# Kernel optimization log

Measured on AMD Instinct MI355X. Metric: run time of the kernel, lower is better.

The kernel has to match this reference:

```python
import math
import jax, jax.numpy as jnp
import numpy as np

HID = 2048
H = 16
HKV = 8
D = HID // H          # 128 head_dim
F = D                 # feature_dim = head_dim
SEQ = 2048
BATCH = 2
THETA = 10000.0


def setup_inputs() -> dict:
    key = jax.random.key(0)
    ks = jax.random.split(key, 10)
    s = lambda k, shape, scale=0.02: (jax.random.normal(k, shape, dtype=jnp.float32) * scale)
    return {
        "hidden_states": jax.random.normal(ks[0], (BATCH, SEQ, HID), dtype=jnp.float32),
        "Wq": s(ks[1], (HID, HID)),
        "bq": s(ks[2], (HID,)),
        "Wk": s(ks[3], (HKV * D, HID)),
        "bk": s(ks[4], (HKV * D,)),
        "Wv": s(ks[5], (HKV * D, HID)),
        "bv": s(ks[6], (HKV * D,)),
        "Wo": s(ks[7], (HID, HID)),
        "bo": s(ks[8], (HID,)),
        "rand_matrix": jax.random.normal(ks[9], (F // 2, D), dtype=jnp.float32),
    }


def _rotate_half(x):
    x1, x2 = x[..., : x.shape[-1] // 2], x[..., x.shape[-1] // 2 :]
    return jnp.concatenate((-x2, x1), axis=-1)


def _softmax_kernel(x, R):
    # L2-normalize last dim (norm clamped at 1e-6), project, [sin, cos] features
    n = jnp.sqrt(jnp.sum(x * x, axis=-1, keepdims=True))
    x = x / jnp.maximum(n, 1e-6)
    p = jnp.einsum("...d,ed->...e", x, R)          # [..., F/2]
    feats = jnp.concatenate([jnp.sin(p), jnp.cos(p)], axis=-1)
    return feats / math.sqrt(F)


def reference(hidden_states, Wq, bq, Wk, bk, Wv, bv, Wo, bo, rand_matrix):
    b, s, _ = hidden_states.shape
    q = (hidden_states @ Wq.T + bq).reshape(b, s, H, D).transpose(0, 2, 1, 3)    # bhsd
    k = (hidden_states @ Wk.T + bk).reshape(b, s, HKV, D).transpose(0, 2, 1, 3)
    v = (hidden_states @ Wv.T + bv).reshape(b, s, HKV, D).transpose(0, 2, 1, 3)

    # RoPE (default position_ids = arange)
    inv_freq = 1.0 / (THETA ** (jnp.arange(0, D, 2, dtype=jnp.float32) / D))     # [D/2]
    freqs = jnp.arange(s, dtype=jnp.float32)[:, None] * inv_freq[None, :]        # [s, D/2]
    emb = jnp.concatenate((freqs, freqs), axis=-1)                               # [s, D]
    cos = jnp.cos(emb)[None, None, :, :]
    sin = jnp.sin(emb)[None, None, :, :]
    q = q * cos + _rotate_half(q) * sin
    k = k * cos + _rotate_half(k) * sin

    # GQA repeat (repeat_interleave along head axis)
    rep = H // HKV
    k = jnp.repeat(k, rep, axis=1)
    v = jnp.repeat(v, rep, axis=1)

    qp = _softmax_kernel(q, rand_matrix)   # [b,H,s,F]
    kp = _softmax_kernel(k, rand_matrix)   # [b,H,s,F]

    # Faithful to source einsums: contraction over the HEAD axis
    # torch: 'bsnd,bsnh->bndh' with tensors laid out (b, head, seq, dim)
    kv = jnp.einsum("bhsf,bhsd->bsfd", kp, v)        # [b, s, F, D]
    out = jnp.einsum("bhsf,bsfd->bhsd", qp, kv)      # [b, H, s, D]
    out = out.reshape(b, s, HID)                      # flat reshape, as in source
    return out @ Wo.T + bo
```

## Files before the change

kernel.cpp:

```cpp
#include <hip/hip_runtime.h>
#include <stdint.h>

typedef unsigned short ushort_t;
typedef __bf16 bf16x8 __attribute__((ext_vector_type(8)));
typedef float f32x4 __attribute__((ext_vector_type(4)));
typedef unsigned int u32;

__device__ __forceinline__ float bf2f(ushort_t u) {
    union { u32 u; float f; } x; x.u = ((u32)u) << 16; return x.f;
}
__device__ __forceinline__ ushort_t f2bf(float f) {
    union { float f; u32 u; } x; x.f = f;
    u32 r = x.u + 0x7FFFu + ((x.u >> 16) & 1u);
    return (ushort_t)(r >> 16);
}

__device__ __forceinline__ void async16(const void* gp, void* lp) {
    __builtin_amdgcn_global_load_lds(
        (const __attribute__((address_space(1))) u32*)(gp),
        (__attribute__((address_space(3))) u32*)(lp),
        16, 0, 0);
}

template<int N>
__device__ __forceinline__ void wait_barrier() {
    asm volatile("s_waitcnt vmcnt(%0)\n\ts_barrier" :: "n"(N) : "memory");
}

__global__ __launch_bounds__(256) void cast_all_kernel(
    const float* __restrict__ hs, const float* __restrict__ Wq,
    const float* __restrict__ Wk, const float* __restrict__ Wv,
    const float* __restrict__ Wo, const float* __restrict__ Rm,
    const float* __restrict__ bq, const float* __restrict__ bk,
    const float* __restrict__ bv,
    ushort_t* __restrict__ Xb, ushort_t* __restrict__ Wcat,
    ushort_t* __restrict__ Wo16, ushort_t* __restrict__ Rbf,
    float* __restrict__ bcat)
{
    int bid = blockIdx.x;
    if (bid == 10244) {
        for (int i = threadIdx.x; i < 4096; i += 256) {
            float v = (i < 2048) ? bq[i] : (i < 3072) ? bk[i - 2048] : bv[i - 3072];
            bcat[i] = v;
        }
        return;
    }
    const float* src; ushort_t* dst; int base;
    if (bid < 4096)       { src = hs; dst = Xb;              base = bid; }
    else if (bid < 6144)  { src = Wq; dst = Wcat;            base = bid - 4096; }
    else if (bid < 7168)  { src = Wk; dst = Wcat + 4194304;  base = bid - 6144; }
    else if (bid < 8192)  { src = Wv; dst = Wcat + 6291456;  base = bid - 7168; }
    else if (bid < 10240) { src = Wo; dst = Wo16;            base = bid - 8192; }
    else                  { src = Rm; dst = Rbf;             base = bid - 10240; }
    int i = base * 2048 + threadIdx.x * 8;
    float4 v0 = *reinterpret_cast<const float4*>(src + i);
    float4 v1 = *reinterpret_cast<const float4*>(src + i + 4);
    ushort_t o[8];
    o[0] = f2bf(v0.x); o[1] = f2bf(v0.y); o[2] = f2bf(v0.z); o[3] = f2bf(v0.w);
    o[4] = f2bf(v1.x); o[5] = f2bf(v1.y); o[6] = f2bf(v1.z); o[7] = f2bf(v1.w);
    *reinterpret_cast<uint4*>(dst + i) = *reinterpret_cast<const uint4*>(o);
}

#define CLOSE_PLAIN __builtin_amdgcn_s_barrier()
#define CLOSE_VM(nn) do { asm volatile("s_waitcnt vmcnt(%0)" :: "n"(nn) : "memory"); \
                          __builtin_amdgcn_s_barrier(); } while (0)

template<int BM, int MBLK, int NBLK, int KC, bool STORE_BF16>
__global__ __launch_bounds__(512, 2) void gemm8p_kernel(
    const ushort_t* __restrict__ A, const ushort_t* __restrict__ B,
    const float* __restrict__ bias, void* __restrict__ C,
    const int M, const int N)
{
    constexpr int NT  = KC / 64;
    constexpr int NI  = NT / 2;
    constexpr int MF2 = BM / 64;
    constexpr int NFR = BM / 32;
    constexpr int AH  = BM * 64;
    constexpr int SH  = BM / 128;
    constexpr int BUF = 2 * AH + 32768;
    constexpr int TI  = 2 * SH + 4;
    static_assert(NT % 2 == 0 && NI >= 3, "need even NT >= 6");
    __shared__ alignas(16) char lds[2 * BUF];

    const int tid  = threadIdx.x;
    const int wid  = tid >> 6;
    const int lane = tid & 63;
    const int wm = wid >> 2, wn = wid & 3;

    constexpr int XN  = NBLK / 8;
    constexpr int NXR = 8 / XN;
    constexpr int RH  = MBLK / NXR;
    const int x  = blockIdx.x & 7;
    const int kb = blockIdx.x >> 3;
    const int mb = (x % NXR) * RH + (kb >> 3);
    const int nb = (x / NXR) * 8 + (kb & 7);
    const int am0 = mb * BM, bn0 = nb * 256;

    const int sr3 = tid >> 3;
    const int c8  = tid & 7;
    const int cs  = c8 ^ (sr3 & 7);
    const long K2 = (long)KC * 2;
    const char* agp = (const char*)A + (size_t)(am0 + sr3) * K2 + cs * 16;
    const char* bgp = (const char*)B + (size_t)(bn0 + sr3) * K2 + cs * 16;
    const int ldsw = wid << 10;

    const int fr = lane & 15, fc = lane >> 4;
    const int sw0 = ((fc)     ^ (fr & 7)) * 16;
    const int sw1 = ((4 + fc) ^ (fr & 7)) * 16;
    const int abase = wm * AH + fr * 128;
    const int bbase = 2 * AH + wn * 8192 + fr * 128;

    f32x4 acc[NFR][4] = {};
    bf16x8 bf[4];

    auto stage_half = [&](const char* gp, int rowoff, int bufb, int off,
                          long kof, int niss) {
        char* lp = lds + bufb + off + ldsw;
        const char* g = gp + (size_t)rowoff * K2 + kof;
#pragma unroll
        for (int i = 0; i < niss; ++i)
            async16(g + (size_t)(i * 64) * K2, lp + i * 8192);
    };
#define SA0(T) stage_half(agp, 0,      ((T) & 1) * BUF, 0,          (long)(T) * 128, SH)
#define SA1(T) stage_half(agp, BM / 2, ((T) & 1) * BUF, AH,         (long)(T) * 128, SH)
#define SB0(T) stage_half(bgp, 0,      ((T) & 1) * BUF, 2 * AH,     (long)(T) * 128, 2)
#define SB1(T) stage_half(bgp, 128,    ((T) & 1) * BUF, 2 * AH + 16384, (long)(T) * 128, 2)

#define PH(h, kc, bufb, STG, CLOSE) do {                                      \
    const char* lp_ = lds + (bufb);                                           \
    const int sw_ = (kc) ? sw1 : sw0;                                         \
    if ((h) == 0) {                                                           \
        _Pragma("unroll") for (int n = 0; n < 4; ++n)                         \
            bf[n] = *(const bf16x8*)(lp_ + bbase + n * 2048 + sw_);           \
    }                                                                         \
    bf16x8 af_[MF2];                                                          \
    _Pragma("unroll") for (int j = 0; j < MF2; ++j)                           \
        af_[j] = *(const bf16x8*)(lp_ + abase + ((h) * MF2 + j) * 2048 + sw_);\
    STG;                                                                      \
    __builtin_amdgcn_s_barrier();                                             \
    asm volatile("s_waitcnt lgkmcnt(0)" ::: "memory");                        \
    __builtin_amdgcn_s_setprio(1);                                            \
    _Pragma("unroll") for (int j = 0; j < MF2; ++j)                           \
    _Pragma("unroll") for (int n = 0; n < 4; ++n)                             \
        acc[(h) * MF2 + j][n] = __builtin_amdgcn_mfma_f32_16x16x32_bf16(      \
            af_[j], bf[n], acc[(h) * MF2 + j][n], 0, 0, 0);                   \
    __builtin_amdgcn_s_setprio(0);                                            \
    CLOSE;                                                                    \
} while (0)

    SA0(0); SA1(0); SB0(0); SB1(0);
    SA0(1); SA1(1); SB0(1); SB1(1);
    wait_barrier<TI>();

    PH(0, 0, 0,    (void)0,  CLOSE_PLAIN);
    PH(1, 0, 0,    (void)0,  CLOSE_PLAIN);
    PH(0, 1, 0,    (void)0,  CLOSE_PLAIN);
    PH(1, 1, 0,    SB0(2),   CLOSE_VM(2));
    PH(0, 0, BUF,  SB1(2),   CLOSE_PLAIN);
    PH(1, 0, BUF,  SA0(2),   CLOSE_PLAIN);
    PH(0, 1, BUF,  SA1(2),   CLOSE_PLAIN);
    PH(1, 1, BUF,  SB0(3),   CLOSE_VM(2));

    for (int i = 1; i <= NI - 2; ++i) {
        const int t = 2 * i;
        PH(0, 0, 0,    SB1(t + 1), CLOSE_PLAIN);
        PH(1, 0, 0,    SA0(t + 1), CLOSE_PLAIN);
        PH(0, 1, 0,    SA1(t + 1), CLOSE_PLAIN);
        PH(1, 1, 0,    SB0(t + 2), CLOSE_VM(2));
        PH(0, 0, BUF,  SB1(t + 2), CLOSE_PLAIN);
        PH(1, 0, BUF,  SA0(t + 2), CLOSE_PLAIN);
        PH(0, 1, BUF,  SA1(t + 2), CLOSE_PLAIN);
        PH(1, 1, BUF,  SB0(t + 3), CLOSE_VM(2));
    }

    {
        constexpr int T1 = NT - 1;
        PH(0, 0, 0,    SB1(T1),  CLOSE_PLAIN);
        PH(1, 0, 0,    SA0(T1),  CLOSE_PLAIN);
        PH(0, 1, 0,    SA1(T1),  CLOSE_PLAIN);
        PH(1, 1, 0,    (void)0,  CLOSE_VM(0));
        PH(0, 0, BUF,  (void)0,  CLOSE_PLAIN);
        PH(1, 0, BUF,  (void)0,  CLOSE_PLAIN);
        PH(0, 1, BUF,  (void)0,  CLOSE_PLAIN);
        PH(1, 1, BUF,  (void)0,  CLOSE_PLAIN);
    }

    const int crow0 = fc << 2;
#pragma unroll
    for (int m = 0; m < NFR; ++m) {
        const int row_b = am0 + wm * (BM / 2) + m * 16 + crow0;
#pragma unroll
        for (int n = 0; n < 4; ++n) {
            const int col = bn0 + wn * 64 + n * 16 + fr;
            const float bs = bias[col];
#pragma unroll
            for (int r = 0; r < 4; ++r) {
                const float v = acc[m][n][r] + bs;
                if (STORE_BF16)
                    ((ushort_t*)C)[(size_t)(row_b + r) * N + col] = f2bf(v);
                else
                    ((float*)C)[(size_t)(row_b + r) * N + col] = v;
            }
        }
    }
#undef PH
#undef SA0
#undef SA1
#undef SB0
#undef SB1
}

__global__ __launch_bounds__(256) void fused_attn_kernel(
    const ushort_t* __restrict__ qkv, const ushort_t* __restrict__ Rbf,
    ushort_t* __restrict__ ctx)
{
    __shared__ ushort_t xnb[32][136];
    __shared__ ushort_t fpb[32][136];
    __shared__ float vsm[8][132];
    __shared__ float Am[16][20];

    const int tok = blockIdx.x;
    const int b = tok >> 11, s = tok & 2047;
    const int tid = threadIdx.x;
    const int wid = tid >> 6, lane = tid & 63;
    const ushort_t* row = qkv + (size_t)tok * 4096;

    float invf = exp2f(-(float)lane * (13.287712379549449f / 64.0f));
    float ang = (float)s * invf;
    float sn, cs;
    __sincosf(ang, &sn, &cs);
#pragma unroll
    for (int i = 0; i < 6; ++i) {
        int vec = wid * 6 + i;
        int base = (vec < 16) ? vec * 128 : 2048 + (vec - 16) * 128;
        float a = bf2f(row[base + lane]);
        float c = bf2f(row[base + lane + 64]);
        float ra = a * cs - c * sn;
        float rc = c * cs + a * sn;
        float ss2 = ra * ra + rc * rc;
#pragma unroll
        for (int off = 32; off; off >>= 1) ss2 += __shfl_xor(ss2, off);
        float inv = 1.0f / fmaxf(sqrtf(ss2), 1e-6f);
        xnb[vec][lane]      = f2bf(ra * inv);
        xnb[vec][lane + 64] = f2bf(rc * inv);
    }
    for (int idx = tid; idx < 1024; idx += 256)
        vsm[idx >> 7][idx & 127] = bf2f(row[3072 + idx]);
    __syncthreads();

    {
        const int fr = lane & 15, fc = lane >> 4;
        f32x4 pacc[2] = {};
#pragma unroll
        for (int kc = 0; kc < 4; ++kc) {
            bf16x8 bfrag = *reinterpret_cast<const bf16x8*>(
                Rbf + (wid * 16 + fr) * 128 + kc * 32 + fc * 8);
            bf16x8 a0 = *reinterpret_cast<const bf16x8*>(&xnb[fr][kc * 32 + fc * 8]);
            bf16x8 a1 = *reinterpret_cast<const bf16x8*>(&xnb[16 + fr][kc * 32 + fc * 8]);
            pacc[0] = __builtin_amdgcn_mfma_f32_16x16x32_bf16(a0, bfrag, pacc[0], 0, 0, 0);
            pacc[1] = __builtin_amdgcn_mfma_f32_16x16x32_bf16(a1, bfrag, pacc[1], 0, 0, 0);
        }
        const int e = wid * 16 + fr;
#pragma unroll
        for (int m = 0; m < 2; ++m) {
            if (m == 1 && fc >= 2) break;
#pragma unroll
            for (int r = 0; r < 4; ++r) {
                int vec = m * 16 + fc * 4 + r;
                float sp, cp;
                __sincosf(pacc[m][r], &sp, &cp);
                fpb[vec][e]      = f2bf(sp * 0.08838834764831845f);
                fpb[vec][e + 64] = f2bf(cp * 0.08838834764831845f);
            }
        }
    }
    __syncthreads();

    if (wid == 0) {
        const int fr = lane & 15, fc = lane >> 4;
        f32x4 aacc = {};
#pragma unroll
        for (int kc = 0; kc < 4; ++kc) {
            bf16x8 qa = *reinterpret_cast<const bf16x8*>(&fpb[fr][kc * 32 + fc * 8]);
            bf16x8 ka = *reinterpret_cast<const bf16x8*>(&fpb[16 + fr][kc * 32 + fc * 8]);
            aacc = __builtin_amdgcn_mfma_f32_16x16x32_bf16(qa, ka, aacc, 0, 0, 0);
        }
        if (fr < 8)
#pragma unroll
            for (int r = 0; r < 4; ++r)
                Am[fc * 4 + r][fr] = 2.0f * aacc[r];
    }
    __syncthreads();

    for (int g = tid; g < 512; g += 256) {
        int h = g >> 5;
        int d0 = (g & 31) << 2;
        float4 a = make_float4(0.f, 0.f, 0.f, 0.f);
#pragma unroll
        for (int hk = 0; hk < 8; ++hk) {
            float am = Am[h][hk];
            float4 v = *reinterpret_cast<const float4*>(&vsm[hk][d0]);
            a.x = fmaf(am, v.x, a.x); a.y = fmaf(am, v.y, a.y);
            a.z = fmaf(am, v.z, a.z); a.w = fmaf(am, v.w, a.w);
        }
        int orow = (b << 11) + (h << 7) + (s >> 4);
        int ocol = ((s & 15) << 7) + d0;
        ushort4 o;
        o.x = f2bf(a.x); o.y = f2bf(a.y); o.z = f2bf(a.z); o.w = f2bf(a.w);
        *reinterpret_cast<ushort4*>(&ctx[(size_t)orow * 2048 + ocol]) = o;
    }
}

extern "C" void kernel_launch(void* const* d_in, const int* in_sizes, int n_in,
                              void* d_out, int out_size, void* d_ws, size_t ws_size,
                              hipStream_t stream)
{
    const float* hs = (const float*)d_in[0];
    const float* Wq = (const float*)d_in[1];
    const float* bq = (const float*)d_in[2];
    const float* Wk = (const float*)d_in[3];
    const float* bk = (const float*)d_in[4];
    const float* Wv = (const float*)d_in[5];
    const float* bv = (const float*)d_in[6];
    const float* Wo = (const float*)d_in[7];
    const float* bo = (const float*)d_in[8];
    const float* Rm = (const float*)d_in[9];
    float* out = (float*)d_out;

    char* ws = (char*)d_ws;
    ushort_t* Xb   = (ushort_t*)(ws);
    ushort_t* Wcat = (ushort_t*)(ws + 16777216);
    ushort_t* Wo16 = (ushort_t*)(ws + 33554432);
    ushort_t* qkv  = (ushort_t*)(ws + 41943040);
    ushort_t* ctx  = (ushort_t*)(ws + 75497472);
    float*    bcat = (float*)   (ws + 92274688);
    ushort_t* Rbf  = (ushort_t*)(ws + 92291072);

    cast_all_kernel<<<10245, 256, 0, stream>>>(hs, Wq, Wk, Wv, Wo, Rm,
                                               bq, bk, bv,
                                               Xb, Wcat, Wo16, Rbf, bcat);

    gemm8p_kernel<256, 16, 16, 2048, true><<<256, 512, 0, stream>>>(
        Xb, Wcat, bcat, qkv, 4096, 4096);

    fused_attn_kernel<<<4096, 256, 0, stream>>>(qkv, Rbf, ctx);

    gemm8p_kernel<128, 32, 8, 2048, false><<<256, 512, 0, stream>>>(
        ctx, Wo16, bo, out, 4096, 2048);
}
```

Baseline: 140.4 us.

## Double-buffer LDS fragment reads in registers to overlap with MFMA in GEMM

Restructures the GEMM main loop so that A and B fragments are read from LDS into two register sets (X/Y) one phase ahead of the MFMA block that uses them. It drops the per-phase barrier and lgkmcnt(0) wait that sat before each MFMA block, and adds sched_barrier fences to keep the ordering. The aim is to hide LDS read latency behind matrix instructions and cut synchronization stalls. In exchange it raises VGPR pressure under the 512x2 launch bounds, which risks spills or lower occupancy.

```diff
diff --git a/kernel.cpp b/kernel.cpp
--- a/kernel.cpp
+++ b/kernel.cpp
@@ -64,9 +64,10 @@
 #define CLOSE_PLAIN __builtin_amdgcn_s_barrier()
 #define CLOSE_VM(nn) do { asm volatile("s_waitcnt vmcnt(%0)" :: "n"(nn) : "memory"); \
                           __builtin_amdgcn_s_barrier(); } while (0)
+#define SBAR __builtin_amdgcn_sched_barrier(0)
 
 template<int BM, int MBLK, int NBLK, int KC, bool STORE_BF16>
-__global__ __launch_bounds__(512, 2) void gemm8p_kernel(
+__global__ __launch_bounds__(512, 2) void gemm8r_kernel(
     const ushort_t* __restrict__ A, const ushort_t* __restrict__ B,
     const float* __restrict__ bias, void* __restrict__ C,
     const int M, const int N)
@@ -111,7 +112,7 @@
     const int bbase = 2 * AH + wn * 8192 + fr * 128;
 
     f32x4 acc[NFR][4] = {};
-    bf16x8 bf[4];
+    bf16x8 afX[MF2], afY[MF2], bfX[4], bfY[4];
 
     auto stage_half = [&](const char* gp, int rowoff, int bufb, int off,
                           long kof, int niss) {
@@ -126,63 +127,64 @@
 #define SB0(T) stage_half(bgp, 0,      ((T) & 1) * BUF, 2 * AH,     (long)(T) * 128, 2)
 #define SB1(T) stage_half(bgp, 128,    ((T) & 1) * BUF, 2 * AH + 16384, (long)(T) * 128, 2)
 
-#define PH(h, kc, bufb, STG, CLOSE) do {                                      \
-    const char* lp_ = lds + (bufb);                                           \
-    const int sw_ = (kc) ? sw1 : sw0;                                         \
-    if ((h) == 0) {                                                           \
-        _Pragma("unroll") for (int n = 0; n < 4; ++n)                         \
-            bf[n] = *(const bf16x8*)(lp_ + bbase + n * 2048 + sw_);           \
-    }                                                                         \
-    bf16x8 af_[MF2];                                                          \
-    _Pragma("unroll") for (int j = 0; j < MF2; ++j)                           \
-        af_[j] = *(const bf16x8*)(lp_ + abase + ((h) * MF2 + j) * 2048 + sw_);\
-    STG;                                                                      \
-    __builtin_amdgcn_s_barrier();                                             \
-    asm volatile("s_waitcnt lgkmcnt(0)" ::: "memory");                        \
-    __builtin_amdgcn_s_setprio(1);                                            \
-    _Pragma("unroll") for (int j = 0; j < MF2; ++j)                           \
-    _Pragma("unroll") for (int n = 0; n < 4; ++n)                             \
-        acc[(h) * MF2 + j][n] = __builtin_amdgcn_mfma_f32_16x16x32_bf16(      \
-            af_[j], bf[n], acc[(h) * MF2 + j][n], 0, 0, 0);                   \
-    __builtin_amdgcn_s_setprio(0);                                            \
-    CLOSE;                                                                    \
+    auto rdA = [&](bf16x8 (&dst)[MF2], int bufb, int h, int kc) {
+        const char* lp_ = lds + bufb;
+        const int sw_ = kc ? sw1 : sw0;
+#pragma unroll
+        for (int j = 0; j < MF2; ++j)
+            dst[j] = *(const bf16x8*)(lp_ + abase + (h * MF2 + j) * 2048 + sw_);
+    };
+    auto rdB = [&](bf16x8 (&dst)[4], int bufb, int kc) {
+        const char* lp_ = lds + bufb;
+        const int sw_ = kc ? sw1 : sw0;
+#pragma unroll
+        for (int n = 0; n < 4; ++n)
+            dst[n] = *(const bf16x8*)(lp_ + bbase + n * 2048 + sw_);
+    };
+    auto domf = [&](bf16x8 (&af)[MF2], bf16x8 (&bf)[4], int h) {
+        __builtin_amdgcn_s_setprio(1);
+#pragma unroll
+        for (int j = 0; j < MF2; ++j)
+#pragma unroll
+            for (int n = 0; n < 4; ++n)
+                acc[h * MF2 + j][n] = __builtin_amdgcn_mfma_f32_16x16x32_bf16(
+                    af[j], bf[n], acc[h * MF2 + j][n], 0, 0, 0);
+        __builtin_amdgcn_s_setprio(0);
+    };
+
+#define QT(b, S0, C0, S1, C1, S2, C2, S3, C3) do {                 \
+    rdA(afX, b, 0, 0); rdB(bfX, b, 0); rdA(afY, b, 1, 0);          \
+    S0; SBAR; domf(afX, bfX, 0); C0;                               \
+    rdA(afX, b, 0, 1); rdB(bfY, b, 1);                             \
+    S1; SBAR; domf(afY, bfX, 1); C1;                               \
+    rdA(afY, b, 1, 1);                                             \
+    S2; SBAR; domf(afX, bfY, 0); C2;                               \
+    S3; SBAR; domf(afY, bfY, 1); C3;                               \
 } while (0)
 
     SA0(0); SA1(0); SB0(0); SB1(0);
     SA0(1); SA1(1); SB0(1); SB1(1);
     wait_barrier<TI>();
 
-    PH(0, 0, 0,    (void)0,  CLOSE_PLAIN);
-    PH(1, 0, 0,    (void)0,  CLOSE_PLAIN);
-    PH(0, 1, 0,    (void)0,  CLOSE_PLAIN);
-    PH(1, 1, 0,    SB0(2),   CLOSE_VM(2));
-    PH(0, 0, BUF,  SB1(2),   CLOSE_PLAIN);
-    PH(1, 0, BUF,  SA0(2),   CLOSE_PLAIN);
-    PH(0, 1, BUF,  SA1(2),   CLOSE_PLAIN);
-    PH(1, 1, BUF,  SB0(3),   CLOSE_VM(2));
+    QT(0,   (void)0, CLOSE_PLAIN, (void)0, CLOSE_PLAIN,
+            (void)0, CLOSE_PLAIN, SB0(2),  CLOSE_VM(2));
+    QT(BUF, SB1(2),  CLOSE_PLAIN, SA0(2),  CLOSE_PLAIN,
+            SA1(2),  CLOSE_PLAIN, SB0(3),  CLOSE_VM(2));
 
     for (int i = 1; i <= NI - 2; ++i) {
         const int t = 2 * i;
-        PH(0, 0, 0,    SB1(t + 1), CLOSE_PLAIN);
-        PH(1, 0, 0,    SA0(t + 1), CLOSE_PLAIN);
-        PH(0, 1, 0,    SA1(t + 1), CLOSE_PLAIN);
-        PH(1, 1, 0,    SB0(t + 2), CLOSE_VM(2));
-        PH(0, 0, BUF,  SB1(t + 2), CLOSE_PLAIN);
-        PH(1, 0, BUF,  SA0(t + 2), CLOSE_PLAIN);
-        PH(0, 1, BUF,  SA1(t + 2), CLOSE_PLAIN);
-        PH(1, 1, BUF,  SB0(t + 3), CLOSE_VM(2));
+        QT(0,   SB1(t + 1), CLOSE_PLAIN, SA0(t + 1), CLOSE_PLAIN,
+                SA1(t + 1), CLOSE_PLAIN, SB0(t + 2), CLOSE_VM(2));
+        QT(BUF, SB1(t + 2), CLOSE_PLAIN, SA0(t + 2), CLOSE_PLAIN,
+                SA1(t + 2), CLOSE_PLAIN, SB0(t + 3), CLOSE_VM(2));
     }
 
     {
         constexpr int T1 = NT - 1;
-        PH(0, 0, 0,    SB1(T1),  CLOSE_PLAIN);
-        PH(1, 0, 0,    SA0(T1),  CLOSE_PLAIN);
-        PH(0, 1, 0,    SA1(T1),  CLOSE_PLAIN);
-        PH(1, 1, 0,    (void)0,  CLOSE_VM(0));
-        PH(0, 0, BUF,  (void)0,  CLOSE_PLAIN);
-        PH(1, 0, BUF,  (void)0,  CLOSE_PLAIN);
-        PH(0, 1, BUF,  (void)0,  CLOSE_PLAIN);
-        PH(1, 1, BUF,  (void)0,  CLOSE_PLAIN);
+        QT(0,   SB1(T1), CLOSE_PLAIN, SA0(T1), CLOSE_PLAIN,
+                SA1(T1), CLOSE_PLAIN, (void)0, CLOSE_VM(0));
+        QT(BUF, (void)0, CLOSE_PLAIN, (void)0, CLOSE_PLAIN,
+                (void)0, CLOSE_PLAIN, (void)0, CLOSE_PLAIN);
     }
 
     const int crow0 = fc << 2;
@@ -203,7 +205,7 @@
             }
         }
     }
-#undef PH
+#undef QT
 #undef SA0
 #undef SA1
 #undef SB0
@@ -340,11 +342,11 @@
                                                bq, bk, bv,
                                                Xb, Wcat, Wo16, Rbf, bcat);
 
-    gemm8p_kernel<256, 16, 16, 2048, true><<<256, 512, 0, stream>>>(
+    gemm8r_kernel<256, 16, 16, 2048, true><<<256, 512, 0, stream>>>(
         Xb, Wcat, bcat, qkv, 4096, 4096);
 
     fused_attn_kernel<<<4096, 256, 0, stream>>>(qkv, Rbf, ctx);
 
-    gemm8p_kernel<128, 32, 8, 2048, false><<<256, 512, 0, stream>>>(
+    gemm8r_kernel<128, 32, 8, 2048, false><<<256, 512, 0, stream>>>(
         ctx, Wo16, bo, out, 4096, 2048);
 }
```

Result: no change. 140.8 us (+0.3%).

## Add 32x32x16 MFMA GEMM variant with wider warp tiles for QKV projection

Applied to the files above, without the earlier changes.

Adds a new GEMM kernel that uses 32x32x16 bf16 MFMA instructions with 16-element accumulators and a restructured per-warp fragment layout. It keeps the half-step pipelined LDS staging and swaps it in for the fused QKV projection GEMM. The larger MFMA tile is meant to cut LDS fragment reads per flop and raise matrix-core throughput. The cost is higher accumulator register pressure. The epilogue also stores scattered bf16 values element by element, which may write less efficiently.

```diff
diff --git a/kernel.cpp b/kernel.cpp
--- a/kernel.cpp
+++ b/kernel.cpp
@@ -4,6 +4,7 @@
 typedef unsigned short ushort_t;
 typedef __bf16 bf16x8 __attribute__((ext_vector_type(8)));
 typedef float f32x4 __attribute__((ext_vector_type(4)));
+typedef float f32x16 __attribute__((ext_vector_type(16)));
 typedef unsigned int u32;
 
 __device__ __forceinline__ float bf2f(ushort_t u) {
@@ -64,6 +65,157 @@
 #define CLOSE_PLAIN __builtin_amdgcn_s_barrier()
 #define CLOSE_VM(nn) do { asm volatile("s_waitcnt vmcnt(%0)" :: "n"(nn) : "memory"); \
                           __builtin_amdgcn_s_barrier(); } while (0)
+
+template<int BM, int MBLK, int NBLK, int KC, bool STORE_BF16>
+__global__ __launch_bounds__(512, 2) void gemm8w_kernel(
+    const ushort_t* __restrict__ A, const ushort_t* __restrict__ B,
+    const float* __restrict__ bias, void* __restrict__ C,
+    const int M, const int N)
+{
+    constexpr int NT  = KC / 64;
+    constexpr int NI  = NT / 2;
+    constexpr int MT  = BM / 64;
+    constexpr int MTH = MT / 2;
+    constexpr int AH  = BM * 64;
+    constexpr int SH  = BM / 128;
+    constexpr int BUF = 2 * AH + 32768;
+    constexpr int TI  = 2 * SH + 4;
+    static_assert(NT % 2 == 0 && NI >= 3 && MTH >= 1, "geometry");
+    __shared__ alignas(16) char lds[2 * BUF];
+
+    const int tid  = threadIdx.x;
+    const int wid  = tid >> 6;
+    const int lane = tid & 63;
+    const int wm = wid >> 2, wn = wid & 3;
+
+    constexpr int XN  = NBLK / 8;
+    constexpr int NXR = 8 / XN;
+    constexpr int RH  = MBLK / NXR;
+    const int x  = blockIdx.x & 7;
+    const int kb = blockIdx.x >> 3;
+    const int mb = (x % NXR) * RH + (kb >> 3);
+    const int nb = (x / NXR) * 8 + (kb & 7);
+    const int am0 = mb * BM, bn0 = nb * 256;
+
+    const int sr3 = tid >> 3;
+    const int c8  = tid & 7;
+    const int cs  = c8 ^ (sr3 & 7);
+    const long K2 = (long)KC * 2;
+    const char* agp = (const char*)A + (size_t)(am0 + sr3) * K2 + cs * 16;
+    const char* bgp = (const char*)B + (size_t)(bn0 + sr3) * K2 + cs * 16;
+    const int ldsw = wid << 10;
+
+    const int fr32 = lane & 31, fc2 = lane >> 5;
+    int swk[4];
+#pragma unroll
+    for (int ks = 0; ks < 4; ++ks)
+        swk[ks] = ((ks * 2 + fc2) ^ (fr32 & 7)) * 16;
+    const int abase = wm * AH + fr32 * 128;
+    const int bbase = 2 * AH + wn * 8192 + fr32 * 128;
+
+    f32x16 acc[MT][2] = {};
+    bf16x8 bfv[2][2];
+
+    auto stage_half = [&](const char* gp, int rowoff, int bufb, int off,
+                          long kof, int niss) {
+        char* lp = lds + bufb + off + ldsw;
+        const char* g = gp + (size_t)rowoff * K2 + kof;
+#pragma unroll
+        for (int i = 0; i < niss; ++i)
+            async16(g + (size_t)(i * 64) * K2, lp + i * 8192);
+    };
+#define WSA0(T) stage_half(agp, 0,      ((T) & 1) * BUF, 0,          (long)(T) * 128, SH)
+#define WSA1(T) stage_half(agp, BM / 2, ((T) & 1) * BUF, AH,         (long)(T) * 128, SH)
+#define WSB0(T) stage_half(bgp, 0,      ((T) & 1) * BUF, 2 * AH,     (long)(T) * 128, 2)
+#define WSB1(T) stage_half(bgp, 128,    ((T) & 1) * BUF, 2 * AH + 16384, (long)(T) * 128, 2)
+
+#define PHW(h, kc, bufb, STG, CLOSE) do {                                     \
+    const char* lp_ = lds + (bufb);                                           \
+    if ((h) == 0) {                                                           \
+        _Pragma("unroll") for (int nt = 0; nt < 2; ++nt)                      \
+        _Pragma("unroll") for (int kl = 0; kl < 2; ++kl)                      \
+            bfv[nt][kl] = *(const bf16x8*)(lp_ + bbase + nt * 4096            \
+                                           + swk[(kc) * 2 + kl]);             \
+    }                                                                         \
+    bf16x8 af_[MTH][2];                                                       \
+    _Pragma("unroll") for (int j = 0; j < MTH; ++j)                           \
+    _Pragma("unroll") for (int kl = 0; kl < 2; ++kl)                          \
+        af_[j][kl] = *(const bf16x8*)(lp_ + abase                             \
+                        + ((h) * MTH + j) * 4096 + swk[(kc) * 2 + kl]);       \
+    STG;                                                                      \
+    __builtin_amdgcn_s_barrier();                                             \
+    asm volatile("s_waitcnt lgkmcnt(0)" ::: "memory");                        \
+    __builtin_amdgcn_s_setprio(1);                                            \
+    _Pragma("unroll") for (int kl = 0; kl < 2; ++kl)                          \
+    _Pragma("unroll") for (int j = 0; j < MTH; ++j)                           \
+    _Pragma("unroll") for (int nt = 0; nt < 2; ++nt)                          \
+        acc[(h) * MTH + j][nt] = __builtin_amdgcn_mfma_f32_32x32x16_bf16(     \
+            af_[j][kl], bfv[nt][kl], acc[(h) * MTH + j][nt], 0, 0, 0);        \
+    __builtin_amdgcn_s_setprio(0);                                            \
+    CLOSE;                                                                    \
+} while (0)
+
+    WSA0(0); WSA1(0); WSB0(0); WSB1(0);
+    WSA0(1); WSA1(1); WSB0(1); WSB1(1);
+    wait_barrier<TI>();
+
+    PHW(0, 0, 0,    (void)0,  CLOSE_PLAIN);
+    PHW(1, 0, 0,    (void)0,  CLOSE_PLAIN);
+    PHW(0, 1, 0,    (void)0,  CLOSE_PLAIN);
+    PHW(1, 1, 0,    WSB0(2),  CLOSE_VM(2));
+    PHW(0, 0, BUF,  WSB1(2),  CLOSE_PLAIN);
+    PHW(1, 0, BUF,  WSA0(2),  CLOSE_PLAIN);
+    PHW(0, 1, BUF,  WSA1(2),  CLOSE_PLAIN);
+    PHW(1, 1, BUF,  WSB0(3),  CLOSE_VM(2));
+
+    for (int i = 1; i <= NI - 2; ++i) {
+        const int t = 2 * i;
+        PHW(0, 0, 0,    WSB1(t + 1), CLOSE_PLAIN);
+        PHW(1, 0, 0,    WSA0(t + 1), CLOSE_PLAIN);
+        PHW(0, 1, 0,    WSA1(t + 1), CLOSE_PLAIN);
+        PHW(1, 1, 0,    WSB0(t + 2), CLOSE_VM(2));
+        PHW(0, 0, BUF,  WSB1(t + 2), CLOSE_PLAIN);
+        PHW(1, 0, BUF,  WSA0(t + 2), CLOSE_PLAIN);
+        PHW(0, 1, BUF,  WSA1(t + 2), CLOSE_PLAIN);
+        PHW(1, 1, BUF,  WSB0(t + 3), CLOSE_VM(2));
+    }
+
+    {
+        constexpr int T1 = NT - 1;
+        PHW(0, 0, 0,    WSB1(T1),  CLOSE_PLAIN);
+        PHW(1, 0, 0,    WSA0(T1),  CLOSE_PLAIN);
+        PHW(0, 1, 0,    WSA1(T1),  CLOSE_PLAIN);
+        PHW(1, 1, 0,    (void)0,   CLOSE_VM(0));
+        PHW(0, 0, BUF,  (void)0,   CLOSE_PLAIN);
+        PHW(1, 0, BUF,  (void)0,   CLOSE_PLAIN);
+        PHW(0, 1, BUF,  (void)0,   CLOSE_PLAIN);
+        PHW(1, 1, BUF,  (void)0,   CLOSE_PLAIN);
+    }
+
+#pragma unroll
+    for (int mt = 0; mt < MT; ++mt) {
+        const int rowb = am0 + wm * (BM / 2) + mt * 32 + fc2 * 4;
+#pragma unroll
+        for (int nt = 0; nt < 2; ++nt) {
+            const int col = bn0 + wn * 64 + nt * 32 + fr32;
+            const float bs = bias[col];
+#pragma unroll
+            for (int r = 0; r < 16; ++r) {
+                const int row = rowb + (r & 3) + 8 * (r >> 2);
+                const float v = acc[mt][nt][r] + bs;
+                if (STORE_BF16)
+                    ((ushort_t*)C)[(size_t)row * N + col] = f2bf(v);
+                else
+                    ((float*)C)[(size_t)row * N + col] = v;
+            }
+        }
+    }
+#undef PHW
+#undef WSA0
+#undef WSA1
+#undef WSB0
+#undef WSB1
+}
 
 template<int BM, int MBLK, int NBLK, int KC, bool STORE_BF16>
 __global__ __launch_bounds__(512, 2) void gemm8p_kernel(
@@ -340,7 +492,7 @@
                                                bq, bk, bv,
                                                Xb, Wcat, Wo16, Rbf, bcat);
 
-    gemm8p_kernel<256, 16, 16, 2048, true><<<256, 512, 0, stream>>>(
+    gemm8w_kernel<256, 16, 16, 2048, true><<<256, 512, 0, stream>>>(
         Xb, Wcat, bcat, qkv, 4096, 4096);
 
     fused_attn_kernel<<<4096, 256, 0, stream>>>(qkv, Rbf, ctx);
```

Measured after the change: 146.4 us. 4.3% more time.
